# Kernel optimization log

Hardware: AMD Instinct MI355X
Metric: run time of the kernel (lower is better)

The kernel has to match this reference:

```python
import jax, jax.numpy as jnp
import numpy as np

B = 8192
N_CLASSES = 10

_AX = 'abcd'
_CNOT = jnp.array([[1, 0, 0, 0], [0, 1, 0, 0], [0, 0, 0, 1], [0, 0, 1, 0]], jnp.float32).reshape(2, 2, 2, 2)


def _ry(theta):
    c, s = jnp.cos(theta / 2), jnp.sin(theta / 2)
    return jnp.stack([jnp.stack([c, -s]), jnp.stack([s, c])])  # [2,2]


def _ap1(state, U, w):
    # apply single-qubit gate U on wire w; state: [N,2,2,2,2]
    i = _AX[:w] + 'i' + _AX[w + 1:]
    o = _AX[:w] + 'o' + _AX[w + 1:]
    return jnp.einsum(f'oi,n{i}->n{o}', U, state)


def _ap2(state, U, w0, w1):
    # apply two-qubit gate U [2,2,2,2]=(out0,out1,in0,in1) on wires (w0,w1)
    i, o = list(_AX), list(_AX)
    i[w0], i[w1] = 'i', 'j'
    o[w0], o[w1] = 'o', 'p'
    return jnp.einsum(f"opij,n{''.join(i)}->n{''.join(o)}", U, state)


def quantum_features(data, q_params):
    # data: [N,4] RY encoding angles applied to |0000>
    h = data / 2
    v = jnp.stack([jnp.cos(h), jnp.sin(h)], -1)  # [N,4,2]
    state = jnp.einsum('na,nb,nc,nd->nabcd', v[:, 0], v[:, 1], v[:, 2], v[:, 3])
    # fixed 8-op random layer instance (real-valued): 5 RY + 3 CNOT
    state = _ap1(state, _ry(q_params[0]), 0)
    state = _ap1(state, _ry(q_params[1]), 1)
    state = _ap2(state, _CNOT, 0, 1)
    state = _ap1(state, _ry(q_params[2]), 2)
    state = _ap1(state, _ry(q_params[3]), 3)
    state = _ap2(state, _CNOT, 2, 3)
    state = _ap1(state, _ry(q_params[4]), 1)
    state = _ap2(state, _CNOT, 1, 2)
    probs = state * state  # real statevector -> |amp|^2
    sgn = jnp.array([1.0, -1.0], jnp.float32)
    z = jnp.stack([
        jnp.einsum('nabcd,a->n', probs, sgn),
        jnp.einsum('nabcd,b->n', probs, sgn),
        jnp.einsum('nabcd,c->n', probs, sgn),
        jnp.einsum('nabcd,d->n', probs, sgn)], -1)
    return z  # [N,4] PauliZ expectations


def setup_inputs() -> dict:
    key = jax.random.key(0)
    ks = jax.random.split(key, 6)
    return {
        'x': jax.random.normal(ks[0], (B, 1, 28, 28), jnp.float32),
        'conv_w': jax.random.normal(ks[1], (4, 1, 2, 2), jnp.float32) * 0.5,
        'conv_b': jax.random.normal(ks[2], (4,), jnp.float32) * 0.1,
        'q_params': jax.random.uniform(ks[3], (5,), jnp.float32, 0.0, 2.0 * np.pi),
        'lin_w': jax.random.normal(ks[4], (N_CLASSES, 1568), jnp.float32) * 0.02,
        'lin_b': jnp.zeros((N_CLASSES,), jnp.float32),
    }


def reference(x, conv_w, conv_b, q_params, lin_w, lin_b):
    feats = jax.lax.conv_general_dilated(
        x, conv_w, window_strides=(2, 2), padding='VALID',
        dimension_numbers=('NCHW', 'OIHW', 'NCHW')) + conv_b[None, :, None, None]
    bsz = feats.shape[0]
    flat = feats.reshape(bsz, -1)  # [B,784]
    # extractor views flat as [B,28,28] and takes 2x2 patches -> [B*196,4]
    patches = flat.reshape(bsz, 14, 2, 14, 2).transpose(0, 1, 3, 2, 4).reshape(bsz * 196, 4)
    q = quantum_features(patches, q_params).reshape(bsz, 784)
    combined = jnp.concatenate([flat, q], axis=1)  # [B,1568]
    logits = combined @ lin_w.T + lin_b
    return jax.nn.log_softmax(logits, axis=-1)
```

## Files before the change

### kernel.cpp

```cpp
#include <hip/hip_runtime.h>
#include <hip/hip_bf16.h>


#define SPB 4
#define THREADS 256
#define NCLS 10
#define FEAT 1568

__global__ __launch_bounds__(THREADS, 6)
void quanv_fused_kernel(const float* __restrict__ x,
                        const float* __restrict__ conv_w,
                        const float* __restrict__ conv_b,
                        const float* __restrict__ q_params,
                        const float* __restrict__ lin_w,
                        const float* __restrict__ lin_b,
                        float* __restrict__ out)
{
    __shared__ float comb[SPB][FEAT];

    const int tid = threadIdx.x;
    const int n0  = blockIdx.x * SPB;

    float W[4][4], Bc[4];
    #pragma unroll
    for (int c = 0; c < 4; ++c) {
        #pragma unroll
        for (int k = 0; k < 4; ++k) W[c][k] = conv_w[c * 4 + k];
        Bc[c] = conv_b[c];
    }
    const float qp0 = q_params[0], qp1 = q_params[1];
    const float qp2 = q_params[2], qp3 = q_params[3];
    const float q4  = q_params[4];
    const float cq4 = __cosf(q4), sq4 = __sinf(q4);

    for (int p = tid; p < SPB * 14 * 7; p += THREADS) {
        const int s = p / 98, t = p % 98;
        const int h = t / 7, wp = t % 7;
        const float* xp = x + (size_t)(n0 + s) * 784 + 56 * h + 4 * wp;
        const float4 r0 = *reinterpret_cast<const float4*>(xp);
        const float4 r1 = *reinterpret_cast<const float4*>(xp + 28);
        const int r = h * 14 + 2 * wp;
        #pragma unroll
        for (int c = 0; c < 4; ++c) {
            comb[s][c * 196 + r] =
                fmaf(r0.x, W[c][0], fmaf(r0.y, W[c][1],
                fmaf(r1.x, W[c][2], fmaf(r1.y, W[c][3], Bc[c]))));
            comb[s][c * 196 + r + 1] =
                fmaf(r0.z, W[c][0], fmaf(r0.w, W[c][1],
                fmaf(r1.z, W[c][2], fmaf(r1.w, W[c][3], Bc[c]))));
        }
    }
    __syncthreads();

    for (int p = tid; p < SPB * 196; p += THREADS) {
        const int s = p / 196, r = p % 196;
        const int i = r / 14, j = r % 14;
        const int base = 56 * i + 2 * j;
        const float2 d01 = *reinterpret_cast<const float2*>(&comb[s][base]);
        const float2 d23 = *reinterpret_cast<const float2*>(&comb[s][base + 28]);
        const float a0 = d01.x + qp0, a1 = d01.y + qp1;
        const float a2 = d23.x + qp2, a3 = d23.y + qp3;
        const float c0 = __cosf(a0);
        const float c1 = __cosf(a1), s1 = __sinf(a1);
        const float c2 = __cosf(a2), c3 = __cosf(a3);
        const float z0 = c0;
        const float z1 = cq4 * c0 * c1 - sq4 * s1;
        const float z2 = z1 * c2;
        const float z3 = c2 * c3;
        *reinterpret_cast<float4*>(&comb[s][784 + r * 4]) =
            make_float4(z0, z1, z2, z3);
    }
    __syncthreads();

    const int wave = tid >> 6, lane = tid & 63;
    const int s = wave;

    float acc[NCLS];
    #pragma unroll
    for (int c = 0; c < NCLS; ++c) acc[c] = 0.f;

    #pragma unroll
    for (int kb = 0; kb < 6; ++kb) {
        const int k = kb * 256 + lane * 4;
        const float4 v = *reinterpret_cast<const float4*>(&comb[s][k]);
        #pragma unroll
        for (int c = 0; c < NCLS; ++c) {
            const float4 w4 = *reinterpret_cast<const float4*>(&lin_w[c * FEAT + k]);
            acc[c] = fmaf(v.x, w4.x, fmaf(v.y, w4.y,
                     fmaf(v.z, w4.z, fmaf(v.w, w4.w, acc[c]))));
        }
    }
    if (lane < 32) {
        const int k = 1536 + lane;
        const float v = comb[s][k];
        #pragma unroll
        for (int c = 0; c < NCLS; ++c)
            acc[c] = fmaf(v, lin_w[c * FEAT + k], acc[c]);
    }

    #pragma unroll
    for (int m = 1; m < 64; m <<= 1) {
        #pragma unroll
        for (int c = 0; c < NCLS; ++c)
            acc[c] += __shfl_xor(acc[c], m, 64);
    }

    if (lane == 0) {
        float lg[NCLS], mx = -1e30f;
        #pragma unroll
        for (int c = 0; c < NCLS; ++c) {
            lg[c] = acc[c] + lin_b[c];
            mx = fmaxf(mx, lg[c]);
        }
        float sum = 0.f;
        #pragma unroll
        for (int c = 0; c < NCLS; ++c) sum += __expf(lg[c] - mx);
        const float lse = mx + __logf(sum);
        float* o = out + (size_t)(n0 + s) * NCLS;
        #pragma unroll
        for (int c = 0; c < NCLS; ++c) o[c] = lg[c] - lse;
    }
}

extern "C" void kernel_launch(void* const* d_in, const int* in_sizes, int n_in,
                              void* d_out, int out_size, void* d_ws, size_t ws_size,
                              hipStream_t stream) {
    const float* x        = (const float*)d_in[0];
    const float* conv_w   = (const float*)d_in[1];
    const float* conv_b   = (const float*)d_in[2];
    const float* q_params = (const float*)d_in[3];
    const float* lin_w    = (const float*)d_in[4];
    const float* lin_b    = (const float*)d_in[5];
    float* out = (float*)d_out;

    const int B = in_sizes[0] / 784;
    const int nblocks = B / SPB;

    quanv_fused_kernel<<<nblocks, THREADS, 0, stream>>>(
        x, conv_w, conv_b, q_params, lin_w, lin_b, out);
}
```

Before: 103.0 us.

## Store features in fp16 LDS and compute linear layer with MFMA

Intermediate conv and quantum features are stored in shared memory as fp16 instead of fp32, halving LDS footprint so occupancy can rise (launch bounds raised to 8). The final 1568x10 linear layer is recast as 16x16x32 f16 MFMA tiles split across the four waves along K, with partial sums combined through a small shared buffer instead of per-wave shuffle reductions. This removes the many scalar FMAs and butterfly shuffles, but wastes most of the MFMA tile (only 4 samples by 10 classes are used). It also lowers precision of activations and weights to fp16.

```diff
diff --git a/kernel.cpp b/kernel.cpp
--- a/kernel.cpp
+++ b/kernel.cpp
@@ -1,5 +1,6 @@
 #include <hip/hip_runtime.h>
 #include <hip/hip_bf16.h>
+#include <hip/hip_fp16.h>
 
 
 #define SPB 4
@@ -7,7 +8,10 @@
 #define NCLS 10
 #define FEAT 1568
 
-__global__ __launch_bounds__(THREADS, 6)
+typedef _Float16 half8 __attribute__((ext_vector_type(8)));
+typedef float f32x4 __attribute__((ext_vector_type(4)));
+
+__global__ __launch_bounds__(THREADS, 8)
 void quanv_fused_kernel(const float* __restrict__ x,
                         const float* __restrict__ conv_w,
                         const float* __restrict__ conv_b,
@@ -16,7 +20,8 @@
                         const float* __restrict__ lin_b,
                         float* __restrict__ out)
 {
-    __shared__ float comb[SPB][FEAT];
+    __shared__ __attribute__((aligned(16))) __half comb[SPB][FEAT];
+    __shared__ float partC[4][4][16];
 
     const int tid = threadIdx.x;
     const int n0  = blockIdx.x * SPB;
@@ -42,12 +47,14 @@
         const int r = h * 14 + 2 * wp;
         #pragma unroll
         for (int c = 0; c < 4; ++c) {
-            comb[s][c * 196 + r] =
+            const float v0 =
                 fmaf(r0.x, W[c][0], fmaf(r0.y, W[c][1],
                 fmaf(r1.x, W[c][2], fmaf(r1.y, W[c][3], Bc[c]))));
-            comb[s][c * 196 + r + 1] =
+            const float v1 =
                 fmaf(r0.z, W[c][0], fmaf(r0.w, W[c][1],
                 fmaf(r1.z, W[c][2], fmaf(r1.w, W[c][3], Bc[c]))));
+            *reinterpret_cast<__half2*>(&comb[s][c * 196 + r]) =
+                __floats2half2_rn(v0, v1);
         }
     }
     __syncthreads();
@@ -56,8 +63,10 @@
         const int s = p / 196, r = p % 196;
         const int i = r / 14, j = r % 14;
         const int base = 56 * i + 2 * j;
-        const float2 d01 = *reinterpret_cast<const float2*>(&comb[s][base]);
-        const float2 d23 = *reinterpret_cast<const float2*>(&comb[s][base + 28]);
+        const float2 d01 = __half22float2(
+            *reinterpret_cast<const __half2*>(&comb[s][base]));
+        const float2 d23 = __half22float2(
+            *reinterpret_cast<const __half2*>(&comb[s][base + 28]));
         const float a0 = d01.x + qp0, a1 = d01.y + qp1;
         const float a2 = d23.x + qp2, a3 = d23.y + qp3;
         const float c0 = __cosf(a0);
@@ -67,49 +76,49 @@
         const float z1 = cq4 * c0 * c1 - sq4 * s1;
         const float z2 = z1 * c2;
         const float z3 = c2 * c3;
-        *reinterpret_cast<float4*>(&comb[s][784 + r * 4]) =
-            make_float4(z0, z1, z2, z3);
+        union { uint2 u; __half2 h[2]; } O;
+        O.h[0] = __floats2half2_rn(z0, z1);
+        O.h[1] = __floats2half2_rn(z2, z3);
+        *reinterpret_cast<uint2*>(&comb[s][784 + r * 4]) = O.u;
     }
     __syncthreads();
 
     const int wave = tid >> 6, lane = tid & 63;
-    const int s = wave;
+    const int l15  = lane & 15;
+    const int srow = (l15 < SPB)  ? l15 : 0;
+    const int wrow = (l15 < NCLS) ? l15 : (NCLS - 1);
+    const int ksub = (lane >> 4) * 8;
 
-    float acc[NCLS];
-    #pragma unroll
-    for (int c = 0; c < NCLS; ++c) acc[c] = 0.f;
-
-    #pragma unroll
-    for (int kb = 0; kb < 6; ++kb) {
-        const int k = kb * 256 + lane * 4;
-        const float4 v = *reinterpret_cast<const float4*>(&comb[s][k]);
-        #pragma unroll
-        for (int c = 0; c < NCLS; ++c) {
-            const float4 w4 = *reinterpret_cast<const float4*>(&lin_w[c * FEAT + k]);
-            acc[c] = fmaf(v.x, w4.x, fmaf(v.y, w4.y,
-                     fmaf(v.z, w4.z, fmaf(v.w, w4.w, acc[c]))));
-        }
-    }
-    if (lane < 32) {
-        const int k = 1536 + lane;
-        const float v = comb[s][k];
-        #pragma unroll
-        for (int c = 0; c < NCLS; ++c)
-            acc[c] = fmaf(v, lin_w[c * FEAT + k], acc[c]);
+    f32x4 acc = {0.f, 0.f, 0.f, 0.f};
+    for (int kc = wave; kc < 49; kc += 4) {
+        const int k0 = kc * 32 + ksub;
+        const half8 a = *reinterpret_cast<const half8*>(&comb[srow][k0]);
+        const float4 w0 =
+            *reinterpret_cast<const float4*>(&lin_w[wrow * FEAT + k0]);
+        const float4 w1 =
+            *reinterpret_cast<const float4*>(&lin_w[wrow * FEAT + k0 + 4]);
+        half8 b;
+        b[0] = (_Float16)w0.x; b[1] = (_Float16)w0.y;
+        b[2] = (_Float16)w0.z; b[3] = (_Float16)w0.w;
+        b[4] = (_Float16)w1.x; b[5] = (_Float16)w1.y;
+        b[6] = (_Float16)w1.z; b[7] = (_Float16)w1.w;
+        acc = __builtin_amdgcn_mfma_f32_16x16x32_f16(a, b, acc, 0, 0, 0);
     }
 
-    #pragma unroll
-    for (int m = 1; m < 64; m <<= 1) {
+    if (lane < 16) {
         #pragma unroll
-        for (int c = 0; c < NCLS; ++c)
-            acc[c] += __shfl_xor(acc[c], m, 64);
+        for (int i = 0; i < 4; ++i)
+            partC[wave][i][lane] = acc[i];
     }
+    __syncthreads();
 
-    if (lane == 0) {
+    if (tid < SPB) {
+        const int s = tid;
         float lg[NCLS], mx = -1e30f;
         #pragma unroll
         for (int c = 0; c < NCLS; ++c) {
-            lg[c] = acc[c] + lin_b[c];
+            lg[c] = partC[0][s][c] + partC[1][s][c] +
+                    partC[2][s][c] + partC[3][s][c] + lin_b[c];
             mx = fmaxf(mx, lg[c]);
         }
         float sum = 0.f;
```

New measurement: 93.03 us. 1.11x faster.
